# Kernel tuning notes

Measured on AMD Instinct MI355X. Metric: run time of the kernel, lower is better.

Reference implementation:

```python
import jax, jax.numpy as jnp
import numpy as np

TMAX = 8
RMS_EPS = 1e-6
PRE_EPS = 0.01
SINKHORN_EPS = 1e-6
POST_MULT = 2.0

HC = 4
C = 2048
K = HC * C            # 8192
OUT = 2 * HC + HC * HC  # 24


def setup_inputs() -> dict:
    key = jax.random.key(0)
    k_x, k_phi, k_b, k1, k2, k3 = jax.random.split(key, 6)
    x = jax.random.normal(k_x, (4, 4096, HC, C), dtype=jnp.float32)
    phi = jax.random.normal(k_phi, (K, OUT), dtype=jnp.float32) * 0.02  # keep logits sane
    b = jax.random.normal(k_b, (OUT,), dtype=jnp.float32) * 0.1
    alpha_pre = jax.random.uniform(k1, (1,), dtype=jnp.float32)
    alpha_post = jax.random.uniform(k2, (1,), dtype=jnp.float32)
    alpha_res = jax.random.uniform(k3, (1,), dtype=jnp.float32)
    return {"x": x, "phi": phi, "b": b, "alpha_pre": alpha_pre,
            "alpha_post": alpha_post, "alpha_res": alpha_res}


def _sinkhorn(logits, tmax, eps):
    # logits: [N, HC, HC]
    mat = jax.nn.softmax(logits, axis=-1) + eps
    mat = mat / (mat.sum(axis=-2, keepdims=True) + eps)
    for _ in range(tmax - 1):  # small fixed trip count
        mat = mat / (mat.sum(axis=-1, keepdims=True) + eps)
        mat = mat / (mat.sum(axis=-2, keepdims=True) + eps)
    return mat


def reference(x, phi, b, alpha_pre, alpha_post, alpha_res):
    hc, c = x.shape[-2], x.shape[-1]
    outer = x.shape[:-2]
    x_mat = x.reshape(-1, hc * c).astype(jnp.float32)          # [N, K]
    invr = jax.lax.rsqrt(jnp.mean(x_mat * x_mat, axis=-1, keepdims=True) + RMS_EPS)
    mix = (x_mat @ phi.astype(jnp.float32)) * invr             # [N, 2*hc + hc*hc]
    h_pre = jax.nn.sigmoid(mix[:, :hc] * alpha_pre + b[:hc]) + PRE_EPS
    h_post = jax.nn.sigmoid(mix[:, hc:2 * hc] * alpha_post + b[hc:2 * hc]) * POST_MULT
    res_logits = mix[:, 2 * hc:].reshape(-1, hc, hc) * alpha_res + b[2 * hc:].reshape(hc, hc)
    h_res = _sinkhorn(res_logits, TMAX, SINKHORN_EPS)
    return (h_pre.reshape(*outer, hc),
            h_post.reshape(*outer, hc),
            h_res.reshape(*outer, hc, hc))
```

## Files before the change

kernel.cpp:

```cpp
#include <hip/hip_runtime.h>
#include <math.h>

#define KDIM 8192
#define HC 4
#define ROWS_PER_BLOCK 16
#define THREADS 256
#define NCHUNK (KDIM / 256)

static __device__ __forceinline__ float f4get(float4 v, int i) {
    return i == 0 ? v.x : i == 1 ? v.y : i == 2 ? v.z : v.w;
}

__global__ __launch_bounds__(THREADS, 2)
void mhc_coeffs_kernel(const float* __restrict__ x,
                       const float* __restrict__ phi,
                       const float* __restrict__ bvec,
                       const float* __restrict__ a_pre,
                       const float* __restrict__ a_post,
                       const float* __restrict__ a_res,
                       float* __restrict__ out, int nrows)
{
    const int lane = threadIdx.x & 63;
    const int w    = threadIdx.x >> 6;
    const int rowbase = blockIdx.x * ROWS_PER_BLOCK + w * 4;

    float acc[4][25];
#pragma unroll
    for (int r = 0; r < 4; ++r)
#pragma unroll
        for (int j = 0; j < 25; ++j) acc[r][j] = 0.f;

    const float4* xp0 = (const float4*)(x + (size_t)(rowbase + 0) * KDIM) + lane;
    const float4* xp1 = (const float4*)(x + (size_t)(rowbase + 1) * KDIM) + lane;
    const float4* xp2 = (const float4*)(x + (size_t)(rowbase + 2) * KDIM) + lane;
    const float4* xp3 = (const float4*)(x + (size_t)(rowbase + 3) * KDIM) + lane;
    const float4* pp = (const float4*)phi + (size_t)lane * 24;

    float4 xc0 = xp0[0], xc1 = xp1[0], xc2 = xp2[0], xc3 = xp3[0];

    auto do_chunk = [&](const float4* pb, float4 v0, float4 v1, float4 v2, float4 v3) {
#pragma unroll
        for (int kk = 0; kk < 4; ++kk) {
            const float x0 = f4get(v0, kk), x1 = f4get(v1, kk);
            const float x2 = f4get(v2, kk), x3 = f4get(v3, kk);
#pragma unroll
            for (int jj = 0; jj < 6; ++jj) {
                const float4 p = pb[kk * 6 + jj];
#pragma unroll
                for (int u = 0; u < 4; ++u) {
                    const float pv = f4get(p, u);
                    const int j = jj * 4 + u;
                    acc[0][j] = fmaf(x0, pv, acc[0][j]);
                    acc[1][j] = fmaf(x1, pv, acc[1][j]);
                    acc[2][j] = fmaf(x2, pv, acc[2][j]);
                    acc[3][j] = fmaf(x3, pv, acc[3][j]);
                }
            }
            acc[0][24] = fmaf(x0, x0, acc[0][24]);
            acc[1][24] = fmaf(x1, x1, acc[1][24]);
            acc[2][24] = fmaf(x2, x2, acc[2][24]);
            acc[3][24] = fmaf(x3, x3, acc[3][24]);
        }
    };

    for (int c = 0; c < NCHUNK - 1; ++c) {
        const int o = (c + 1) * 64;
        float4 xn0 = xp0[o], xn1 = xp1[o], xn2 = xp2[o], xn3 = xp3[o];
        do_chunk(pp + (size_t)c * 1536, xc0, xc1, xc2, xc3);
        xc0 = xn0; xc1 = xn1; xc2 = xn2; xc3 = xn3;
    }
    do_chunk(pp + (size_t)(NCHUNK - 1) * 1536, xc0, xc1, xc2, xc3);

#pragma unroll
    for (int r = 0; r < 4; ++r)
#pragma unroll
        for (int j = 0; j < 25; ++j) {
            float v = acc[r][j];
            v += __shfl_xor(v, 1);
            v += __shfl_xor(v, 2);
            v += __shfl_xor(v, 4);
            v += __shfl_xor(v, 8);
            v += __shfl_xor(v, 16);
            v += __shfl_xor(v, 32);
            acc[r][j] = v;
        }

    const int r = lane >> 4;
    const int e = lane & 15;
    const int row = rowbase + r;

    float rs[25];
#pragma unroll
    for (int j = 0; j < 25; ++j)
        rs[j] = (r == 0) ? acc[0][j] : (r == 1) ? acc[1][j] : (r == 2) ? acc[2][j] : acc[3][j];

    const float invr = 1.0f / sqrtf(rs[24] * (1.0f / (float)KDIM) + 1e-6f);

    float dres = rs[8];
#pragma unroll
    for (int m = 1; m < 16; ++m) dres = (e == m) ? rs[8 + m] : dres;
    const float lg = fmaf(dres * invr, a_res[0], bvec[8 + e]);

    float mx = fmaxf(lg, __shfl_xor(lg, 1));
    mx = fmaxf(mx, __shfl_xor(mx, 2));
    const float ex = expf(lg - mx);
    float sm = ex + __shfl_xor(ex, 1);
    sm += __shfl_xor(sm, 2);
    float mat = ex / sm + 1e-6f;

    float cs = mat + __shfl_xor(mat, 4);
    cs += __shfl_xor(cs, 8);
    mat = mat / (cs + 1e-6f);
#pragma unroll
    for (int t = 0; t < 7; ++t) {
        float rsum = mat + __shfl_xor(mat, 1);
        rsum += __shfl_xor(rsum, 2);
        mat = mat / (rsum + 1e-6f);
        float csum = mat + __shfl_xor(mat, 4);
        csum += __shfl_xor(csum, 8);
        mat = mat / (csum + 1e-6f);
    }
    out[(size_t)nrows * 8 + (size_t)row * 16 + e] = mat;

    if (e < 8) {
        float dpp = rs[0];
#pragma unroll
        for (int m = 1; m < 8; ++m) dpp = (e == m) ? rs[m] : dpp;
        if (e < 4) {
            const float z = fmaf(dpp * invr, a_pre[0], bvec[e]);
            out[(size_t)row * 4 + e] = 1.0f / (1.0f + expf(-z)) + 0.01f;
        } else {
            const float z = fmaf(dpp * invr, a_post[0], bvec[e]);
            out[(size_t)nrows * 4 + (size_t)row * 4 + (e - 4)] = 2.0f / (1.0f + expf(-z));
        }
    }
}

extern "C" void kernel_launch(void* const* d_in, const int* in_sizes, int n_in,
                              void* d_out, int out_size, void* d_ws, size_t ws_size,
                              hipStream_t stream) {
    const float* x     = (const float*)d_in[0];
    const float* phi   = (const float*)d_in[1];
    const float* bvec  = (const float*)d_in[2];
    const float* apre  = (const float*)d_in[3];
    const float* apost = (const float*)d_in[4];
    const float* ares  = (const float*)d_in[5];
    float* out = (float*)d_out;

    const int nrows  = in_sizes[0] / KDIM;
    const int blocks = nrows / ROWS_PER_BLOCK;

    mhc_coeffs_kernel<<<blocks, THREADS, 0, stream>>>(x, phi, bvec, apre, apost, ares, out, nrows);
}
```

Measured before the change: 1.044 ms.

## Stage phi chunks in swizzled double-buffered LDS shared across block waves

Each 256-wide K chunk of phi is now loaded cooperatively by the block into a double-buffered, XOR-swizzled LDS tile, and the four waves read from it instead of each wave fetching phi from global memory. The x reads change from float4 per lane to scalar strided loads with a prefetch one step ahead, and the occupancy hint rises from 2 to 3 blocks per CU. The goal is to cut redundant phi traffic through L2/L1 and hide latency, at the cost of a barrier per chunk, LDS usage and narrower x loads.

```diff
diff --git a/kernel.cpp b/kernel.cpp
--- a/kernel.cpp
+++ b/kernel.cpp
@@ -2,16 +2,14 @@
 #include <math.h>
 
 #define KDIM 8192
-#define HC 4
-#define ROWS_PER_BLOCK 16
 #define THREADS 256
-#define NCHUNK (KDIM / 256)
+#define RPB 16
+#define CHUNK 256
+#define NCHUNK 32
+#define CHUNK_F4 1536
+#define NKQ 128
 
-static __device__ __forceinline__ float f4get(float4 v, int i) {
-    return i == 0 ? v.x : i == 1 ? v.y : i == 2 ? v.z : v.w;
-}
-
-__global__ __launch_bounds__(THREADS, 2)
+__global__ __launch_bounds__(THREADS, 3)
 void mhc_coeffs_kernel(const float* __restrict__ x,
                        const float* __restrict__ phi,
                        const float* __restrict__ bvec,
@@ -20,9 +18,12 @@
                        const float* __restrict__ a_res,
                        float* __restrict__ out, int nrows)
 {
-    const int lane = threadIdx.x & 63;
-    const int w    = threadIdx.x >> 6;
-    const int rowbase = blockIdx.x * ROWS_PER_BLOCK + w * 4;
+    __shared__ float4 ldsA[CHUNK_F4];
+    __shared__ float4 ldsB[CHUNK_F4];
+
+    const int t    = threadIdx.x;
+    const int lane = t & 63;
+    const int rowbase = blockIdx.x * RPB + (t >> 6) * 4;
 
     float acc[4][25];
 #pragma unroll
@@ -30,46 +31,89 @@
 #pragma unroll
         for (int j = 0; j < 25; ++j) acc[r][j] = 0.f;
 
-    const float4* xp0 = (const float4*)(x + (size_t)(rowbase + 0) * KDIM) + lane;
-    const float4* xp1 = (const float4*)(x + (size_t)(rowbase + 1) * KDIM) + lane;
-    const float4* xp2 = (const float4*)(x + (size_t)(rowbase + 2) * KDIM) + lane;
-    const float4* xp3 = (const float4*)(x + (size_t)(rowbase + 3) * KDIM) + lane;
-    const float4* pp = (const float4*)phi + (size_t)lane * 24;
+    int wslot[6];
+#pragma unroll
+    for (int i = 0; i < 6; ++i) {
+        const int t16 = i * 256 + t;
+        const int row = t16 / 6;
+        wslot[i] = ((t16 * 16) ^ ((row & 7) << 4)) >> 4;
+    }
 
-    float4 xc0 = xp0[0], xc1 = xp1[0], xc2 = xp2[0], xc3 = xp3[0];
+    int rbase[6];
+#pragma unroll
+    for (int j = 0; j < 6; ++j)
+        rbase[j] = (((lane * 96) + j * 16) ^ ((lane & 7) << 4)) >> 4;
 
-    auto do_chunk = [&](const float4* pb, float4 v0, float4 v1, float4 v2, float4 v3) {
+    const float4* phi4 = (const float4*)phi;
+
+    const float* xr0 = x + (size_t)(rowbase + 0) * KDIM + lane;
+    const float* xr1 = x + (size_t)(rowbase + 1) * KDIM + lane;
+    const float* xr2 = x + (size_t)(rowbase + 2) * KDIM + lane;
+    const float* xr3 = x + (size_t)(rowbase + 3) * KDIM + lane;
+
+    float4 s0 = phi4[0 * 256 + t];
+    float4 s1 = phi4[1 * 256 + t];
+    float4 s2 = phi4[2 * 256 + t];
+    float4 s3 = phi4[3 * 256 + t];
+    float4 s4 = phi4[4 * 256 + t];
+    float4 s5 = phi4[5 * 256 + t];
+    float xa0 = xr0[0], xa1 = xr1[0], xa2 = xr2[0], xa3 = xr3[0];
+    ldsA[wslot[0]] = s0; ldsA[wslot[1]] = s1; ldsA[wslot[2]] = s2;
+    ldsA[wslot[3]] = s3; ldsA[wslot[4]] = s4; ldsA[wslot[5]] = s5;
+    __syncthreads();
+
+    float4* cur = ldsA;
+    float4* nxt = ldsB;
+
+    for (int c = 0; c < NCHUNK; ++c) {
+        const bool more = (c + 1 < NCHUNK);
+        if (more) {
+            const float4* pc = phi4 + (size_t)(c + 1) * CHUNK_F4;
+            s0 = pc[t];        s1 = pc[256 + t];  s2 = pc[512 + t];
+            s3 = pc[768 + t];  s4 = pc[1024 + t]; s5 = pc[1280 + t];
+        }
 #pragma unroll
-        for (int kk = 0; kk < 4; ++kk) {
-            const float x0 = f4get(v0, kk), x1 = f4get(v1, kk);
-            const float x2 = f4get(v2, kk), x3 = f4get(v3, kk);
+        for (int q = 0; q < 4; ++q) {
+            const int kq = c * 4 + q;
+            float xb0 = 0.f, xb1 = 0.f, xb2 = 0.f, xb3 = 0.f;
+            if (kq + 1 < NKQ) {
+                const int o = (kq + 1) * 64;
+                xb0 = xr0[o]; xb1 = xr1[o]; xb2 = xr2[o]; xb3 = xr3[o];
+            }
 #pragma unroll
-            for (int jj = 0; jj < 6; ++jj) {
-                const float4 p = pb[kk * 6 + jj];
-#pragma unroll
-                for (int u = 0; u < 4; ++u) {
-                    const float pv = f4get(p, u);
-                    const int j = jj * 4 + u;
-                    acc[0][j] = fmaf(x0, pv, acc[0][j]);
-                    acc[1][j] = fmaf(x1, pv, acc[1][j]);
-                    acc[2][j] = fmaf(x2, pv, acc[2][j]);
-                    acc[3][j] = fmaf(x3, pv, acc[3][j]);
-                }
+            for (int j = 0; j < 6; ++j) {
+                const float4 p = cur[rbase[j] + q * 384];
+                const int jb = j * 4;
+                acc[0][jb + 0] = fmaf(xa0, p.x, acc[0][jb + 0]);
+                acc[0][jb + 1] = fmaf(xa0, p.y, acc[0][jb + 1]);
+                acc[0][jb + 2] = fmaf(xa0, p.z, acc[0][jb + 2]);
+                acc[0][jb + 3] = fmaf(xa0, p.w, acc[0][jb + 3]);
+                acc[1][jb + 0] = fmaf(xa1, p.x, acc[1][jb + 0]);
+                acc[1][jb + 1] = fmaf(xa1, p.y, acc[1][jb + 1]);
+                acc[1][jb + 2] = fmaf(xa1, p.z, acc[1][jb + 2]);
+                acc[1][jb + 3] = fmaf(xa1, p.w, acc[1][jb + 3]);
+                acc[2][jb + 0] = fmaf(xa2, p.x, acc[2][jb + 0]);
+                acc[2][jb + 1] = fmaf(xa2, p.y, acc[2][jb + 1]);
+                acc[2][jb + 2] = fmaf(xa2, p.z, acc[2][jb + 2]);
+                acc[2][jb + 3] = fmaf(xa2, p.w, acc[2][jb + 3]);
+                acc[3][jb + 0] = fmaf(xa3, p.x, acc[3][jb + 0]);
+                acc[3][jb + 1] = fmaf(xa3, p.y, acc[3][jb + 1]);
+                acc[3][jb + 2] = fmaf(xa3, p.z, acc[3][jb + 2]);
+                acc[3][jb + 3] = fmaf(xa3, p.w, acc[3][jb + 3]);
             }
-            acc[0][24] = fmaf(x0, x0, acc[0][24]);
-            acc[1][24] = fmaf(x1, x1, acc[1][24]);
-            acc[2][24] = fmaf(x2, x2, acc[2][24]);
-            acc[3][24] = fmaf(x3, x3, acc[3][24]);
+            acc[0][24] = fmaf(xa0, xa0, acc[0][24]);
+            acc[1][24] = fmaf(xa1, xa1, acc[1][24]);
+            acc[2][24] = fmaf(xa2, xa2, acc[2][24]);
+            acc[3][24] = fmaf(xa3, xa3, acc[3][24]);
+            xa0 = xb0; xa1 = xb1; xa2 = xb2; xa3 = xb3;
         }
-    };
-
-    for (int c = 0; c < NCHUNK - 1; ++c) {
-        const int o = (c + 1) * 64;
-        float4 xn0 = xp0[o], xn1 = xp1[o], xn2 = xp2[o], xn3 = xp3[o];
-        do_chunk(pp + (size_t)c * 1536, xc0, xc1, xc2, xc3);
-        xc0 = xn0; xc1 = xn1; xc2 = xn2; xc3 = xn3;
+        if (more) {
+            nxt[wslot[0]] = s0; nxt[wslot[1]] = s1; nxt[wslot[2]] = s2;
+            nxt[wslot[3]] = s3; nxt[wslot[4]] = s4; nxt[wslot[5]] = s5;
+            float4* tmp = cur; cur = nxt; nxt = tmp;
+            __syncthreads();
+        }
     }
-    do_chunk(pp + (size_t)(NCHUNK - 1) * 1536, xc0, xc1, xc2, xc3);
 
 #pragma unroll
     for (int r = 0; r < 4; ++r)
@@ -112,7 +156,7 @@
     cs += __shfl_xor(cs, 8);
     mat = mat / (cs + 1e-6f);
 #pragma unroll
-    for (int t = 0; t < 7; ++t) {
+    for (int it = 0; it < 7; ++it) {
         float rsum = mat + __shfl_xor(mat, 1);
         rsum += __shfl_xor(rsum, 2);
         mat = mat / (rsum + 1e-6f);
@@ -148,7 +192,7 @@
     float* out = (float*)d_out;
 
     const int nrows  = in_sizes[0] / KDIM;
-    const int blocks = nrows / ROWS_PER_BLOCK;
+    const int blocks = nrows / RPB;
 
     mhc_coeffs_kernel<<<blocks, THREADS, 0, stream>>>(x, phi, bvec, apre, apost, ares, out, nrows);
 }
```

New measurement: 1.535 ms. +46.9%, slower.
